# Kernel tuning notes

Measured on AMD Instinct MI355X. Metric: run time of the kernel, lower is better.

## Reference

```python
import jax, jax.numpy as jnp
import numpy as np

ALPHA = 0.2      # LeakyReLU negative slope
BN_EPS = 1e-5    # torch BatchNorm1d default eps

N_NODES = 50000
N_EDGES = 1600000
DIM_IN = 128
DIM_HID = 64
DIM_OUT = 128
NUM_HEADS = 8


def gat_layer(feat, src, dst, W, a, gamma, beta):
    """One GATLayer forward (dropout disabled, BatchNorm in training mode
    i.e. normalized with batch statistics over the node dimension)."""
    n = feat.shape[0]
    dh = W.shape[1]
    msg = feat @ W                                  # [N, dh]
    attn_src = msg @ a[:dh]                         # [N]
    attn_dst = msg @ a[dh:]                         # [N]
    scores = jax.nn.leaky_relu(attn_src[src] + attn_dst[dst], ALPHA)  # [E]
    scores = scores - scores.max()                  # global max-subtract (as in source)
    e = jnp.exp(scores)                             # [E]
    denom = jax.ops.segment_sum(e, dst, num_segments=n) + 1e-10       # [N]
    coef = e / denom[dst]                           # [E] segment-softmax
    out = jax.ops.segment_sum(msg[src] * coef[:, None], dst, num_segments=n)  # [N, dh]
    # BatchNorm1d (training-mode batch stats, biased variance)
    mean = out.mean(axis=0)
    var = out.var(axis=0)
    out = (out - mean) * jax.lax.rsqrt(var + BN_EPS) * gamma + beta
    return out


def setup_inputs() -> dict:
    key = jax.random.key(0)
    ks = jax.random.split(key, 10)
    feat = jax.random.normal(ks[0], (N_NODES, DIM_IN), dtype=jnp.float32)
    edges = jax.random.randint(ks[1], (2, N_EDGES), 0, N_NODES)

    def xavier(k, shape):
        fan_in, fan_out = shape[0], shape[-1]
        lim = np.sqrt(6.0 / (fan_in + fan_out)).astype(np.float32)
        return jax.random.uniform(k, shape, jnp.float32, -lim, lim)

    W_heads = xavier(ks[2], (NUM_HEADS, DIM_IN, DIM_HID))
    a_heads = xavier(ks[3], (NUM_HEADS, 2 * DIM_HID))
    gamma_h = jnp.ones((NUM_HEADS, DIM_HID), jnp.float32)
    beta_h = jnp.zeros((NUM_HEADS, DIM_HID), jnp.float32)
    W_out = xavier(ks[4], (NUM_HEADS * DIM_HID, DIM_OUT))
    a_out = xavier(ks[5], (2 * DIM_OUT,))
    gamma_o = jnp.ones((DIM_OUT,), jnp.float32)
    beta_o = jnp.zeros((DIM_OUT,), jnp.float32)
    W_res = xavier(ks[6], (DIM_IN, DIM_OUT))
    b_res = jnp.zeros((DIM_OUT,), jnp.float32)
    return {"feat": feat, "edges": edges, "W_heads": W_heads, "a_heads": a_heads,
            "gamma_h": gamma_h, "beta_h": beta_h, "W_out": W_out, "a_out": a_out,
            "gamma_o": gamma_o, "beta_o": beta_o, "W_res": W_res, "b_res": b_res}


def reference(feat, edges, W_heads, a_heads, gamma_h, beta_h,
              W_out, a_out, gamma_o, beta_o, W_res, b_res):
    src, dst = edges[0], edges[1]
    # python loop over a small fixed number of heads keeps peak memory low
    head_outs = [gat_layer(feat, src, dst, W_heads[h], a_heads[h], gamma_h[h], beta_h[h])
                 for h in range(NUM_HEADS)]
    x = jnp.concatenate(head_outs, axis=-1)          # [N, H*dh]
    x = gat_layer(x, src, dst, W_out, a_out, gamma_o, beta_o)  # [N, dout]
    x = x + feat @ W_res + b_res                     # residual Linear
    return x
```

## Files before the change

kernel.cpp:

```cpp
#include <hip/hip_runtime.h>
#include <math.h>

#define N_NODES 50000
#define N_EDGES 1600000
#define DIM_IN  128
#define DIM_HID 64
#define NHEADS  8
#define HDIM    (NHEADS*DIM_HID)
#define DIM_OUT 128
#define SCBLK   1024
#define HISTBLK 2048
#define NMBLK   64
#define LDK     72
#define INV_N   2e-5f
#define CSBLK   400

typedef __attribute__((ext_vector_type(2))) unsigned short us2;
typedef __attribute__((ext_vector_type(4))) unsigned short us4;
typedef __attribute__((ext_vector_type(8))) unsigned short us8;
typedef __attribute__((ext_vector_type(8))) short bf16x8;
typedef __attribute__((ext_vector_type(4))) float f32x4;

__device__ __forceinline__ float leaky(float x) { return x >= 0.f ? x : 0.2f * x; }
__device__ __forceinline__ float bf2f(unsigned short h) {
  return __uint_as_float(((unsigned)h) << 16);
}
__device__ __forceinline__ unsigned short f2bf(float f) {
  unsigned u = __float_as_uint(f);
  unsigned r = (u + 0x7fffu + ((u >> 16) & 1u)) >> 16;
  return (unsigned short)r;
}
__device__ __forceinline__ float bn_scale(float sum, float sq, float g) {
  float mean = sum * INV_N;
  float var = sq * INV_N - mean * mean;
  return g * rsqrtf(var + 1e-5f);
}

__global__ void prep_kernel(const float* __restrict__ feat, const float* __restrict__ Wh,
                            const float* __restrict__ Wres, const int* __restrict__ edst,
                            unsigned short* __restrict__ feat_bf,
                            unsigned short* __restrict__ Bt1,
                            unsigned short* __restrict__ Btr,
                            int* __restrict__ counts) {
  int b = blockIdx.x;
  if (b < 6250) {
    int i = b * 256 + threadIdx.x;
    float4 v = *reinterpret_cast<const float4*>(&feat[(size_t)i * 4]);
    us4 o;
    o[0] = f2bf(v.x); o[1] = f2bf(v.y); o[2] = f2bf(v.z); o[3] = f2bf(v.w);
    *reinterpret_cast<us4*>(&feat_bf[(size_t)i * 4]) = o;
  } else if (b < 6506) {
    int idx = (b - 6250) * 256 + threadIdx.x;
    int n = idx >> 7, k = idx & 127;
    Bt1[idx] = f2bf(Wh[(n >> 6) * (DIM_IN * DIM_HID) + k * DIM_HID + (n & 63)]);
  } else if (b < 6570) {
    int idx = (b - 6506) * 256 + threadIdx.x;
    int n = idx >> 7, k = idx & 127;
    Btr[idx] = f2bf(Wres[k * DIM_OUT + n]);
  } else {
    int bid = b - 6570;
    for (int e = bid * 256 + threadIdx.x; e < N_EDGES; e += HISTBLK * 256)
      atomicAdd(&counts[edst[e]], 1);
  }
}

__global__ __launch_bounds__(256) void foldw2_kernel(
    const float* __restrict__ W,
    const float* __restrict__ colsum, const float* __restrict__ colsq,
    const float* __restrict__ gamma, const float* __restrict__ beta,
    unsigned short* __restrict__ Bt, float* __restrict__ bias2) {
  int idx = blockIdx.x * 256 + threadIdx.x;
  int n = idx >> 9, k = idx & 511;
  float mean = colsum[k] * INV_N;
  float sc = bn_scale(colsum[k], colsq[k], gamma[k]);
  float w = W[k * DIM_OUT + n];
  Bt[idx] = f2bf(w * sc);
  float shift = beta[k] - mean * sc;
  __shared__ float red[256];
  red[threadIdx.x] = shift * w;
  __syncthreads();
#pragma unroll
  for (int off = 128; off; off >>= 1) {
    if (threadIdx.x < off) red[threadIdx.x] += red[threadIdx.x + off];
    __syncthreads();
  }
  if (threadIdx.x == 0) atomicAdd(&bias2[n], red[0]);
}

__device__ __forceinline__ void gemm_body(
    unsigned short* As, unsigned short* Bs,
    const unsigned short* __restrict__ A, const unsigned short* __restrict__ Bt,
    void* __restrict__ Cout, const float* __restrict__ bias,
    int M, int N, int K, int outbf) {
  const int tid = threadIdx.x;
  const int lane = tid & 63, wid = tid >> 6;
  const int wr = wid >> 1, wc = wid & 1;
  const int l15 = lane & 15, lhi = lane >> 4;
  const int m0 = blockIdx.y * 128, n0 = blockIdx.x * 128;
  const int srow = tid >> 3;
  const int sc8 = (tid - srow) & 7;
  f32x4 acc[4][4];
#pragma unroll
  for (int i = 0; i < 4; ++i)
#pragma unroll
    for (int j = 0; j < 4; ++j) acc[i][j] = f32x4{0.f, 0.f, 0.f, 0.f};

  for (int k0 = 0; k0 < K; k0 += 64) {
    __syncthreads();
#pragma unroll
    for (int p = 0; p < 4; ++p) {
      int row = p * 32 + srow;
      us8 va = {0, 0, 0, 0, 0, 0, 0, 0};
      int gr = m0 + row;
      if (gr < M) va = *reinterpret_cast<const us8*>(&A[(size_t)gr * K + k0 + sc8 * 8]);
      *reinterpret_cast<us8*>(&As[row * LDK + sc8 * 8]) = va;
      us8 vb = {0, 0, 0, 0, 0, 0, 0, 0};
      int gn = n0 + row;
      if (gn < N) vb = *reinterpret_cast<const us8*>(&Bt[(size_t)gn * K + k0 + sc8 * 8]);
      *reinterpret_cast<us8*>(&Bs[row * LDK + sc8 * 8]) = vb;
    }
    __syncthreads();
#pragma unroll
    for (int kk = 0; kk < 2; ++kk) {
      bf16x8 af[4], bfr[4];
#pragma unroll
      for (int i = 0; i < 4; ++i)
        af[i] = *reinterpret_cast<const bf16x8*>(&As[(wr * 64 + i * 16 + l15) * LDK + kk * 32 + lhi * 8]);
#pragma unroll
      for (int j = 0; j < 4; ++j)
        bfr[j] = *reinterpret_cast<const bf16x8*>(&Bs[(wc * 64 + j * 16 + l15) * LDK + kk * 32 + lhi * 8]);
#pragma unroll
      for (int i = 0; i < 4; ++i)
#pragma unroll
        for (int j = 0; j < 4; ++j)
          acc[i][j] = __builtin_amdgcn_mfma_f32_16x16x32_bf16(af[i], bfr[j], acc[i][j], 0, 0, 0);
    }
  }
#pragma unroll
  for (int j = 0; j < 4; ++j) {
    int col = n0 + wc * 64 + j * 16 + l15;
    float bb = bias ? bias[col] : 0.f;
#pragma unroll
    for (int i = 0; i < 4; ++i) {
      f32x4 v = acc[i][j];
#pragma unroll
      for (int t = 0; t < 4; ++t) {
        int row = m0 + wr * 64 + i * 16 + lhi * 4 + t;
        if (row < M) {
          float o = v[t] + bb;
          if (outbf) ((unsigned short*)Cout)[(size_t)row * N + col] = f2bf(o);
          else       ((float*)Cout)[(size_t)row * N + col] = o;
        }
      }
    }
  }
}

__global__ __launch_bounds__(256) void gemm1_attn_kernel(
    const unsigned short* __restrict__ A, const unsigned short* __restrict__ Bt,
    unsigned short* __restrict__ Cout, const float* __restrict__ a_heads,
    float* __restrict__ asrc, float* __restrict__ adst) {
  __shared__ unsigned short As[128 * LDK];
  __shared__ unsigned short Bs[128 * LDK];
  const int M = N_NODES, N = HDIM, K = DIM_IN;
  const int tid = threadIdx.x;
  const int lane = tid & 63, wid = tid >> 6;
  const int wr = wid >> 1, wc = wid & 1;
  const int l15 = lane & 15, lhi = lane >> 4;
  const int m0 = blockIdx.y * 128, n0 = blockIdx.x * 128;
  const int srow = tid >> 3;
  const int sc8 = (tid - srow) & 7;
  f32x4 acc[4][4];
#pragma unroll
  for (int i = 0; i < 4; ++i)
#pragma unroll
    for (int j = 0; j < 4; ++j) acc[i][j] = f32x4{0.f, 0.f, 0.f, 0.f};

  for (int k0 = 0; k0 < K; k0 += 64) {
    __syncthreads();
#pragma unroll
    for (int p = 0; p < 4; ++p) {
      int row = p * 32 + srow;
      us8 va = {0, 0, 0, 0, 0, 0, 0, 0};
      int gr = m0 + row;
      if (gr < M) va = *reinterpret_cast<const us8*>(&A[(size_t)gr * K + k0 + sc8 * 8]);
      *reinterpret_cast<us8*>(&As[row * LDK + sc8 * 8]) = va;
      us8 vb = {0, 0, 0, 0, 0, 0, 0, 0};
      int gn = n0 + row;
      if (gn < N) vb = *reinterpret_cast<const us8*>(&Bt[(size_t)gn * K + k0 + sc8 * 8]);
      *reinterpret_cast<us8*>(&Bs[row * LDK + sc8 * 8]) = vb;
    }
    __syncthreads();
#pragma unroll
    for (int kk = 0; kk < 2; ++kk) {
      bf16x8 af[4], bfr[4];
#pragma unroll
      for (int i = 0; i < 4; ++i)
        af[i] = *reinterpret_cast<const bf16x8*>(&As[(wr * 64 + i * 16 + l15) * LDK + kk * 32 + lhi * 8]);
#pragma unroll
      for (int j = 0; j < 4; ++j)
        bfr[j] = *reinterpret_cast<const bf16x8*>(&Bs[(wc * 64 + j * 16 + l15) * LDK + kk * 32 + lhi * 8]);
#pragma unroll
      for (int i = 0; i < 4; ++i)
#pragma unroll
        for (int j = 0; j < 4; ++j)
          acc[i][j] = __builtin_amdgcn_mfma_f32_16x16x32_bf16(af[i], bfr[j], acc[i][j], 0, 0, 0);
    }
  }
#pragma unroll
  for (int j = 0; j < 4; ++j) {
    int col = n0 + wc * 64 + j * 16 + l15;
#pragma unroll
    for (int i = 0; i < 4; ++i) {
      f32x4 v = acc[i][j];
#pragma unroll
      for (int t = 0; t < 4; ++t) {
        int row = m0 + wr * 64 + i * 16 + lhi * 4 + t;
        if (row < M) Cout[(size_t)row * N + col] = f2bf(v[t]);
      }
    }
  }
  const int h = blockIdx.x * 2 + wc;
  float aS[4], aD[4];
#pragma unroll
  for (int j = 0; j < 4; ++j) {
    aS[j] = a_heads[h * 128 + j * 16 + l15];
    aD[j] = a_heads[h * 128 + 64 + j * 16 + l15];
  }
#pragma unroll
  for (int i = 0; i < 4; ++i) {
#pragma unroll
    for (int t = 0; t < 4; ++t) {
      float s = 0.f, d = 0.f;
#pragma unroll
      for (int j = 0; j < 4; ++j) {
        float v = acc[i][j][t];
        s = fmaf(v, aS[j], s);
        d = fmaf(v, aD[j], d);
      }
      s += __shfl_xor(s, 1, 64); s += __shfl_xor(s, 2, 64);
      s += __shfl_xor(s, 4, 64); s += __shfl_xor(s, 8, 64);
      d += __shfl_xor(d, 1, 64); d += __shfl_xor(d, 2, 64);
      d += __shfl_xor(d, 4, 64); d += __shfl_xor(d, 8, 64);
      int row = m0 + wr * 64 + i * 16 + lhi * 4 + t;
      if (l15 == 0 && row < M) {
        asrc[(size_t)row * 8 + h] = s;
        adst[(size_t)row * 8 + h] = d;
      }
    }
  }
}

__global__ __launch_bounds__(256) void gemm_dual(
    const unsigned short* __restrict__ A0, const unsigned short* __restrict__ Bt0,
    unsigned short* __restrict__ C0, const float* __restrict__ b0,
    const float* __restrict__ a_out, float* __restrict__ asrc, float* __restrict__ adst,
    const unsigned short* __restrict__ A1, const unsigned short* __restrict__ Bt1,
    float* __restrict__ C1, const float* __restrict__ b1) {
  __shared__ unsigned short As[128 * LDK];
  __shared__ unsigned short Bs[128 * LDK];
  if (blockIdx.z == 1) {
    gemm_body(As, Bs, A1, Bt1, C1, b1, N_NODES, DIM_OUT, DIM_IN, 0);
    return;
  }
  const int M = N_NODES, N = DIM_OUT, K = HDIM;
  const int tid = threadIdx.x;
  const int lane = tid & 63, wid = tid >> 6;
  const int wr = wid >> 1, wc = wid & 1;
  const int l15 = lane & 15, lhi = lane >> 4;
  const int m0 = blockIdx.y * 128;
  const int srow = tid >> 3;
  const int sc8 = (tid - srow) & 7;
  f32x4 acc[4][4];
#pragma unroll
  for (int i = 0; i < 4; ++i)
#pragma unroll
    for (int j = 0; j < 4; ++j) acc[i][j] = f32x4{0.f, 0.f, 0.f, 0.f};

  for (int k0 = 0; k0 < K; k0 += 64) {
    __syncthreads();
#pragma unroll
    for (int p = 0; p < 4; ++p) {
      int row = p * 32 + srow;
      us8 va = {0, 0, 0, 0, 0, 0, 0, 0};
      int gr = m0 + row;
      if (gr < M) va = *reinterpret_cast<const us8*>(&A0[(size_t)gr * K + k0 + sc8 * 8]);
      *reinterpret_cast<us8*>(&As[row * LDK + sc8 * 8]) = va;
      us8 vb = {0, 0, 0, 0, 0, 0, 0, 0};
      if (row < N) vb = *reinterpret_cast<const us8*>(&Bt0[(size_t)row * K + k0 + sc8 * 8]);
      *reinterpret_cast<us8*>(&Bs[row * LDK + sc8 * 8]) = vb;
    }
    __syncthreads();
#pragma unroll
    for (int kk = 0; kk < 2; ++kk) {
      bf16x8 af[4], bfr[4];
#pragma unroll
      for (int i = 0; i < 4; ++i)
        af[i] = *reinterpret_cast<const bf16x8*>(&As[(wr * 64 + i * 16 + l15) * LDK + kk * 32 + lhi * 8]);
#pragma unroll
      for (int j = 0; j < 4; ++j)
        bfr[j] = *reinterpret_cast<const bf16x8*>(&Bs[(wc * 64 + j * 16 + l15) * LDK + kk * 32 + lhi * 8]);
#pragma unroll
      for (int i = 0; i < 4; ++i)
#pragma unroll
        for (int j = 0; j < 4; ++j)
          acc[i][j] = __builtin_amdgcn_mfma_f32_16x16x32_bf16(af[i], bfr[j], acc[i][j], 0, 0, 0);
    }
  }
#pragma unroll
  for (int j = 0; j < 4; ++j) {
    int col = wc * 64 + j * 16 + l15;
    float bb = b0[col];
#pragma unroll
    for (int i = 0; i < 4; ++i) {
      f32x4 v = acc[i][j];
#pragma unroll
      for (int t = 0; t < 4; ++t) {
        int row = m0 + wr * 64 + i * 16 + lhi * 4 + t;
        if (row < M) C0[(size_t)row * N + col] = f2bf(v[t] + bb);
      }
    }
  }
  __shared__ float att_sh[2][64][2][2];
  float aS[4], aD[4];
#pragma unroll
  for (int j = 0; j < 4; ++j) {
    int col = wc * 64 + j * 16 + l15;
    float bb = b0[col];
    aS[j] = a_out[col];
    aD[j] = a_out[128 + col];
    (void)bb;
  }
#pragma unroll
  for (int i = 0; i < 4; ++i) {
#pragma unroll
    for (int t = 0; t < 4; ++t) {
      float s = 0.f, d = 0.f;
#pragma unroll
      for (int j = 0; j < 4; ++j) {
        int col = wc * 64 + j * 16 + l15;
        float v = acc[i][j][t] + b0[col];
        s = fmaf(v, aS[j], s);
        d = fmaf(v, aD[j], d);
      }
      s += __shfl_xor(s, 1, 64); s += __shfl_xor(s, 2, 64);
      s += __shfl_xor(s, 4, 64); s += __shfl_xor(s, 8, 64);
      d += __shfl_xor(d, 1, 64); d += __shfl_xor(d, 2, 64);
      d += __shfl_xor(d, 4, 64); d += __shfl_xor(d, 8, 64);
      if (l15 == 0) {
        att_sh[wr][i * 16 + lhi * 4 + t][wc][0] = s;
        att_sh[wr][i * 16 + lhi * 4 + t][wc][1] = d;
      }
    }
  }
  __syncthreads();
  if (tid < 128) {
    int wrr = tid >> 6, r = tid & 63;
    int row = m0 + wrr * 64 + r;
    if (row < M) {
      asrc[row] = att_sh[wrr][r][0][0] + att_sh[wrr][r][1][0];
      adst[row] = att_sh[wrr][r][0][1] + att_sh[wrr][r][1][1];
    }
  }
}

__global__ __launch_bounds__(256) void nodemax_part_kernel(
    const float* __restrict__ a, const float* __restrict__ b,
    float* __restrict__ part, int total) {
  int t = threadIdx.x;
  float ms = -3.4e38f, md = -3.4e38f;
  for (int i = blockIdx.x * 256 + t; i < total; i += NMBLK * 256) {
    ms = fmaxf(ms, a[i]);
    md = fmaxf(md, b[i]);
  }
  ms = fmaxf(ms, __shfl_xor(ms, 8, 64));
  ms = fmaxf(ms, __shfl_xor(ms, 16, 64));
  ms = fmaxf(ms, __shfl_xor(ms, 32, 64));
  md = fmaxf(md, __shfl_xor(md, 8, 64));
  md = fmaxf(md, __shfl_xor(md, 16, 64));
  md = fmaxf(md, __shfl_xor(md, 32, 64));
  __shared__ float sh[4][8][2];
  int wv = t >> 6, ln = t & 63;
  if (ln < 8) { sh[wv][ln][0] = ms; sh[wv][ln][1] = md; }
  __syncthreads();
  if (t < 8) {
    float s4 = fmaxf(fmaxf(sh[0][t][0], sh[1][t][0]), fmaxf(sh[2][t][0], sh[3][t][0]));
    float d4 = fmaxf(fmaxf(sh[0][t][1], sh[1][t][1]), fmaxf(sh[2][t][1], sh[3][t][1]));
    part[blockIdx.x * 16 + t * 2] = s4;
    part[blockIdx.x * 16 + t * 2 + 1] = d4;
  }
}

__global__ void nodemax_final_kernel(const float* __restrict__ part, float* __restrict__ maxv, int H) {
  int t = threadIdx.x;
  int ch = t & 15, k = t >> 4;
  float m = -3.4e38f;
  for (int i = k; i < NMBLK; i += 4) m = fmaxf(m, part[i * 16 + ch]);
  m = fmaxf(m, __shfl_xor(m, 16, 64));
  m = fmaxf(m, __shfl_xor(m, 32, 64));
  float S = __shfl(m, (t & 7) * 2, 64);
  float D = __shfl(m, (t & 7) * 2 + 1, 64);
  if (H == 8) {
    if (t < 8) maxv[t] = S + D;
  } else {
    float Sm = S, Dm = D;
    Sm = fmaxf(Sm, __shfl_xor(Sm, 1, 64)); Sm = fmaxf(Sm, __shfl_xor(Sm, 2, 64));
    Sm = fmaxf(Sm, __shfl_xor(Sm, 4, 64));
    Dm = fmaxf(Dm, __shfl_xor(Dm, 1, 64)); Dm = fmaxf(Dm, __shfl_xor(Dm, 2, 64));
    Dm = fmaxf(Dm, __shfl_xor(Dm, 4, 64));
    if (t == 0) maxv[0] = Sm + Dm;
  }
}

__global__ __launch_bounds__(256) void scan1_kernel(
    const int* __restrict__ counts, int* __restrict__ rowptr, int* __restrict__ bsum, int n) {
  __shared__ int wsum[4];
  int b0 = blockIdx.x * 1024;
  int t = threadIdx.x;
  int lane = t & 63, w = t >> 6;
  int v[4]; int s = 0;
#pragma unroll
  for (int i = 0; i < 4; ++i) {
    int idx = b0 + t * 4 + i;
    v[i] = (idx < n) ? counts[idx] : 0;
    s += v[i];
  }
  int x = s;
#pragma unroll
  for (int off = 1; off < 64; off <<= 1) {
    int y = __shfl_up(x, off, 64);
    if (lane >= off) x += y;
  }
  if (lane == 63) wsum[w] = x;
  __syncthreads();
  int wof = 0;
  for (int i = 0; i < w; ++i) wof += wsum[i];
  int run = wof + x - s;
#pragma unroll
  for (int i = 0; i < 4; ++i) {
    int idx = b0 + t * 4 + i;
    if (idx < n) rowptr[idx] = run;
    run += v[i];
  }
  if (t == 255) bsum[blockIdx.x] = wof + x;
}

__global__ __launch_bounds__(256) void scan23_kernel(
    int* __restrict__ rowptr, const int* __restrict__ bsum, int n) {
  __shared__ int carry_sh;
  int b = blockIdx.x, t = threadIdx.x;
  if (t < 64) {
    int v = (t < b) ? bsum[t] : 0;
#pragma unroll
    for (int off = 32; off; off >>= 1) v += __shfl_xor(v, off, 64);
    if (t == 0) carry_sh = v;
  }
  __syncthreads();
  int carry = carry_sh;
  int i0 = b * 1024;
#pragma unroll
  for (int q = 0; q < 4; ++q) {
    int i = i0 + q * 256 + t;
    if (i < n) rowptr[i] += carry;
  }
  if (b == gridDim.x - 1 && t == 0) rowptr[n] = N_EDGES;
}

__global__ __launch_bounds__(256) void scatter_kernel(
    const int* __restrict__ esrc, const int* __restrict__ edst,
    const int* __restrict__ rowptr, int* __restrict__ cursor,
    int* __restrict__ colsrc, int E) {
  for (int e = blockIdx.x * blockDim.x + threadIdx.x; e < E; e += gridDim.x * blockDim.x) {
    int d = edst[e];
    int pos = rowptr[d] + atomicAdd(&cursor[d], 1);
    colsrc[pos] = esrc[e];
  }
}

__global__ __launch_bounds__(256) void agg1_kernel(
    const unsigned short* __restrict__ msg, const float* __restrict__ asrc,
    const float* __restrict__ adst, const float* __restrict__ maxv,
    const int* __restrict__ rowptr, const int* __restrict__ colsrc,
    unsigned short* __restrict__ out) {
  int wv = threadIdx.x >> 6, l = threadIdx.x & 63;
  int n = blockIdx.x * 4 + wv;
  const int h = l >> 3;
  const int eloc = l & 7;
  const int hbase = l & 56;
  float M = maxv[h];
  float ad = adst[(size_t)n * 8 + h];
  int e0 = rowptr[n], e1 = rowptr[n + 1];
  float acc[8];
#pragma unroll
  for (int j = 0; j < 8; ++j) acc[j] = 0.f;
  float ds = 0.f;
  int base = e0;
  for (; base + 8 <= e1; base += 8) {
    int sreg = colsrc[base + eloc];
    float x = asrc[(size_t)sreg * 8 + h] + ad;
    x = x >= 0.f ? x : 0.2f * x;
    float creg = __expf(x - M);
#pragma unroll
    for (int e = 0; e < 8; ++e) {
      float c = __shfl(creg, hbase | e, 64);
      int s = __shfl(sreg, e, 64);
      ds += c;
      us8 m = *reinterpret_cast<const us8*>(&msg[(size_t)s * HDIM + l * 8]);
#pragma unroll
      for (int j = 0; j < 8; ++j) acc[j] = fmaf(bf2f(m[j]), c, acc[j]);
    }
  }
  if (base < e1) {
    int cnt = e1 - base;
    int sreg = 0; float creg = 0.f;
    if (eloc < cnt) {
      sreg = colsrc[base + eloc];
      float x = asrc[(size_t)sreg * 8 + h] + ad;
      x = x >= 0.f ? x : 0.2f * x;
      creg = __expf(x - M);
    }
    for (int e = 0; e < cnt; ++e) {
      float c = __shfl(creg, hbase | e, 64);
      int s = __shfl(sreg, e, 64);
      ds += c;
      us8 m = *reinterpret_cast<const us8*>(&msg[(size_t)s * HDIM + l * 8]);
#pragma unroll
      for (int j = 0; j < 8; ++j) acc[j] = fmaf(bf2f(m[j]), c, acc[j]);
    }
  }
  float inv = 1.0f / (ds + 1e-10f);
  us8 o;
#pragma unroll
  for (int j = 0; j < 8; ++j) o[j] = f2bf(acc[j] * inv);
  *reinterpret_cast<us8*>(&out[(size_t)n * HDIM + l * 8]) = o;
}

__global__ __launch_bounds__(256) void agg2_kernel(
    const unsigned short* __restrict__ msg, const float* __restrict__ asrc,
    const float* __restrict__ adst, const float* __restrict__ maxv,
    const int* __restrict__ rowptr, const int* __restrict__ colsrc,
    float* __restrict__ out) {
  int wv = threadIdx.x >> 6, ln = threadIdx.x & 63;
  int n = blockIdx.x * 4 + wv;
  float M = maxv[0];
  float ad = adst[n];
  int e0 = rowptr[n], e1 = rowptr[n + 1];
  float a0 = 0.f, a1 = 0.f, ds = 0.f;
  for (int base = e0; base < e1; base += 64) {
    int cnt = min(64, e1 - base);
    int s_reg = 0; float c_reg = 0.f;
    if (ln < cnt) {
      s_reg = colsrc[base + ln];
      float x = asrc[s_reg] + ad;
      x = x >= 0.f ? x : 0.2f * x;
      c_reg = __expf(x - M);
    }
    int e = 0;
    for (; e + 4 <= cnt; e += 4) {
      int s0 = __shfl(s_reg, e, 64),     s1 = __shfl(s_reg, e + 1, 64);
      int s2 = __shfl(s_reg, e + 2, 64), s3 = __shfl(s_reg, e + 3, 64);
      float c0 = __shfl(c_reg, e, 64),     c1 = __shfl(c_reg, e + 1, 64);
      float c2 = __shfl(c_reg, e + 2, 64), c3 = __shfl(c_reg, e + 3, 64);
      us2 m0 = *reinterpret_cast<const us2*>(&msg[(size_t)s0 * 128 + 2 * ln]);
      us2 m1 = *reinterpret_cast<const us2*>(&msg[(size_t)s1 * 128 + 2 * ln]);
      us2 m2 = *reinterpret_cast<const us2*>(&msg[(size_t)s2 * 128 + 2 * ln]);
      us2 m3 = *reinterpret_cast<const us2*>(&msg[(size_t)s3 * 128 + 2 * ln]);
      ds += (c0 + c1) + (c2 + c3);
      a0 = fmaf(bf2f(m0[0]), c0, a0); a1 = fmaf(bf2f(m0[1]), c0, a1);
      a0 = fmaf(bf2f(m1[0]), c1, a0); a1 = fmaf(bf2f(m1[1]), c1, a1);
      a0 = fmaf(bf2f(m2[0]), c2, a0); a1 = fmaf(bf2f(m2[1]), c2, a1);
      a0 = fmaf(bf2f(m3[0]), c3, a0); a1 = fmaf(bf2f(m3[1]), c3, a1);
    }
    for (; e < cnt; ++e) {
      int s = __shfl(s_reg, e, 64);
      float c = __shfl(c_reg, e, 64);
      us2 m = *reinterpret_cast<const us2*>(&msg[(size_t)s * 128 + 2 * ln]);
      ds += c;
      a0 = fmaf(bf2f(m[0]), c, a0);
      a1 = fmaf(bf2f(m[1]), c, a1);
    }
  }
  float inv = 1.0f / (ds + 1e-10f);
  float2 r; r.x = a0 * inv; r.y = a1 * inv;
  *reinterpret_cast<float2*>(&out[(size_t)n * 128 + 2 * ln]) = r;
}

__global__ __launch_bounds__(256) void colstats_bf512_kernel(
    const unsigned short* __restrict__ X, float* __restrict__ sums,
    float* __restrict__ sqs, int M) {
  int tid = threadIdx.x;
  int cg = tid & 63;
  int wv = tid >> 6;
  int rows = (M + gridDim.x - 1) / gridDim.x;
  int r0 = blockIdx.x * rows;
  int r1 = min(M, r0 + rows);
  float s[8], q[8];
#pragma unroll
  for (int j = 0; j < 8; ++j) { s[j] = 0.f; q[j] = 0.f; }
  for (int r = r0 + wv; r < r1; r += 4) {
    us8 v = *reinterpret_cast<const us8*>(&X[(size_t)r * 512 + cg * 8]);
#pragma unroll
    for (int j = 0; j < 8; ++j) {
      float f = bf2f(v[j]);
      s[j] += f; q[j] = fmaf(f, f, q[j]);
    }
  }
  __shared__ float shs[3][512];
  __shared__ float shq[3][512];
  if (wv > 0) {
#pragma unroll
    for (int j = 0; j < 8; ++j) {
      shs[wv - 1][cg * 8 + j] = s[j];
      shq[wv - 1][cg * 8 + j] = q[j];
    }
  }
  __syncthreads();
  if (wv == 0) {
#pragma unroll
    for (int j = 0; j < 8; ++j) {
      int c = cg * 8 + j;
      atomicAdd(&sums[c], s[j] + shs[0][c] + shs[1][c] + shs[2][c]);
      atomicAdd(&sqs[c],  q[j] + shq[0][c] + shq[1][c] + shq[2][c]);
    }
  }
}

__global__ __launch_bounds__(256) void colstats_f128_kernel(
    const float* __restrict__ X, float* __restrict__ sums,
    float* __restrict__ sqs, int M) {
  int tid = threadIdx.x;
  int g = tid & 31;
  int slot = tid >> 5;
  int rows = (M + gridDim.x - 1) / gridDim.x;
  int r0 = blockIdx.x * rows;
  int r1 = min(M, r0 + rows);
  float s[4] = {0.f, 0.f, 0.f, 0.f}, q[4] = {0.f, 0.f, 0.f, 0.f};
  for (int r = r0 + slot; r < r1; r += 8) {
    float4 v = *reinterpret_cast<const float4*>(&X[(size_t)r * 128 + g * 4]);
    s[0] += v.x; q[0] = fmaf(v.x, v.x, q[0]);
    s[1] += v.y; q[1] = fmaf(v.y, v.y, q[1]);
    s[2] += v.z; q[2] = fmaf(v.z, v.z, q[2]);
    s[3] += v.w; q[3] = fmaf(v.w, v.w, q[3]);
  }
#pragma unroll
  for (int j = 0; j < 4; ++j) {
    s[j] += __shfl_xor(s[j], 32, 64);
    q[j] += __shfl_xor(q[j], 32, 64);
  }
  __shared__ float shs[3][128];
  __shared__ float shq[3][128];
  int wv = tid >> 6, ln = tid & 63;
  if (wv > 0 && ln < 32) {
#pragma unroll
    for (int j = 0; j < 4; ++j) {
      shs[wv - 1][g * 4 + j] = s[j];
      shq[wv - 1][g * 4 + j] = q[j];
    }
  }
  __syncthreads();
  if (wv == 0 && ln < 32) {
#pragma unroll
    for (int j = 0; j < 4; ++j) {
      int c = g * 4 + j;
      atomicAdd(&sums[c], s[j] + shs[0][c] + shs[1][c] + shs[2][c]);
      atomicAdd(&sqs[c],  q[j] + shq[0][c] + shq[1][c] + shq[2][c]);
    }
  }
}

__global__ void final_kernel(float* __restrict__ out, const float* __restrict__ resid,
                             const float* __restrict__ colsum, const float* __restrict__ colsq,
                             const float* __restrict__ gamma, const float* __restrict__ beta,
                             int total) {
  for (int i = blockIdx.x * blockDim.x + threadIdx.x; i < total; i += gridDim.x * blockDim.x) {
    int c = i & 127;
    float mean = colsum[c] * INV_N;
    float sc = bn_scale(colsum[c], colsq[c], gamma[c]);
    float sh = beta[c] - mean * sc;
    out[i] = fmaf(out[i], sc, sh) + resid[i];
  }
}

extern "C" void kernel_launch(void* const* d_in, const int* in_sizes, int n_in,
                              void* d_out, int out_size, void* d_ws, size_t ws_size,
                              hipStream_t stream) {
  const float* feat    = (const float*)d_in[0];
  const int*   edges   = (const int*)d_in[1];
  const int*   esrc    = edges;
  const int*   edst    = edges + N_EDGES;
  const float* W_heads = (const float*)d_in[2];
  const float* a_heads = (const float*)d_in[3];
  const float* gamma_h = (const float*)d_in[4];
  const float* beta_h  = (const float*)d_in[5];
  const float* W_out   = (const float*)d_in[6];
  const float* a_out   = (const float*)d_in[7];
  const float* gamma_o = (const float*)d_in[8];
  const float* beta_o  = (const float*)d_in[9];
  const float* W_res   = (const float*)d_in[10];
  const float* b_res   = (const float*)d_in[11];
  float* out = (float*)d_out;

  char* ws = (char*)d_ws;
  size_t off = 0;
  auto alloc = [&](size_t bytes) {
    void* p = ws + off;
    off = (off + bytes + 255) & ~(size_t)255;
    return p;
  };
  unsigned short* msg1    = (unsigned short*)alloc((size_t)N_NODES * HDIM * 2);
  unsigned short* out1_bf = (unsigned short*)alloc((size_t)N_NODES * HDIM * 2);
  unsigned short* feat_bf = (unsigned short*)alloc((size_t)N_NODES * DIM_IN * 2);
  float*    resid  = (float*)alloc((size_t)N_NODES * DIM_OUT * 4);
  float*    asrc1  = (float*)alloc((size_t)N_NODES * NHEADS * 4);
  float*    adst1  = (float*)alloc((size_t)N_NODES * NHEADS * 4);
  int*      counts = (int*)alloc((size_t)N_NODES * 4);
  int*      cursor = (int*)alloc((size_t)N_NODES * 4);
  float*    bias2  = (float*)alloc(DIM_OUT * 4);
  int*      rowptr = (int*)alloc((size_t)(N_NODES + 1) * 4);
  int*      colsrc = (int*)alloc((size_t)N_EDGES * 4);
  int*      bsum   = (int*)alloc(64 * 4);
  float*    partmx = (float*)alloc((size_t)NMBLK * 16 * 4);
  float*    maxv1  = (float*)alloc(8 * 4);
  float*    maxv2  = (float*)alloc(4);
  float*    colsum = (float*)alloc(HDIM * 4);
  float*    colsq  = (float*)alloc(HDIM * 4);
  unsigned short* Bt1 = (unsigned short*)alloc((size_t)HDIM * DIM_IN * 2);
  unsigned short* Bt2 = (unsigned short*)alloc((size_t)DIM_OUT * HDIM * 2);
  unsigned short* Btr = (unsigned short*)alloc((size_t)DIM_OUT * DIM_IN * 2);
  unsigned short* msg2 = msg1;
  float* asrc2 = asrc1; float* adst2 = adst1;
  (void)n_in; (void)in_sizes; (void)out_size; (void)ws_size;

  hipMemsetAsync(counts, 0, (char*)rowptr - (char*)counts, stream);
  hipMemsetAsync(colsum, 0, 4096, stream);

  prep_kernel<<<6570 + HISTBLK, 256, 0, stream>>>(feat, W_heads, W_res, edst,
                                                  feat_bf, Bt1, Btr, counts);

  dim3 g1(HDIM / 128, (N_NODES + 127) / 128);
  gemm1_attn_kernel<<<g1, 256, 0, stream>>>(feat_bf, Bt1, msg1, a_heads, asrc1, adst1);
  nodemax_part_kernel<<<NMBLK, 256, 0, stream>>>(asrc1, adst1, partmx, N_NODES * 8);
  nodemax_final_kernel<<<1, 64, 0, stream>>>(partmx, maxv1, 8);

  int nsb = (N_NODES + 1023) / 1024;
  scan1_kernel<<<nsb, 256, 0, stream>>>(counts, rowptr, bsum, N_NODES);
  scan23_kernel<<<nsb, 256, 0, stream>>>(rowptr, bsum, N_NODES);

  scatter_kernel<<<SCBLK, 256, 0, stream>>>(esrc, edst, rowptr, cursor, colsrc, N_EDGES);
  agg1_kernel<<<N_NODES / 4, 256, 0, stream>>>(msg1, asrc1, adst1, maxv1, rowptr, colsrc, out1_bf);

  colstats_bf512_kernel<<<CSBLK, 256, 0, stream>>>(out1_bf, colsum, colsq, N_NODES);
  foldw2_kernel<<<DIM_OUT * HDIM / 256, 256, 0, stream>>>(W_out, colsum, colsq,
                                                          gamma_h, beta_h, Bt2, bias2);

  dim3 g2d(1, (N_NODES + 127) / 128, 2);
  gemm_dual<<<g2d, 256, 0, stream>>>(out1_bf, Bt2, msg2, bias2, a_out, asrc2, adst2,
                                     feat_bf, Btr, resid, b_res);
  nodemax_part_kernel<<<NMBLK, 256, 0, stream>>>(asrc2, adst2, partmx, N_NODES);
  nodemax_final_kernel<<<1, 64, 0, stream>>>(partmx, maxv2, 1);

  agg2_kernel<<<N_NODES / 4, 256, 0, stream>>>(msg2, asrc2, adst2, maxv2, rowptr, colsrc, out);

  hipMemsetAsync(colsum, 0, 4096, stream);
  colstats_f128_kernel<<<CSBLK, 256, 0, stream>>>(out, colsum, colsq, N_NODES);
  final_kernel<<<2048, 256, 0, stream>>>(out, resid, colsum, colsq, gamma_o, beta_o,
                                         N_NODES * DIM_OUT);
}
```

Measured before the change: 716.8 us.

## Fuse attention max reduction into GEMM epilogues and widen agg2 loads

```diff
diff --git a/kernel.cpp b/kernel.cpp
--- a/kernel.cpp
+++ b/kernel.cpp
@@ -10,7 +10,7 @@
 #define DIM_OUT 128
 #define SCBLK   1024
 #define HISTBLK 2048
-#define NMBLK   64
+#define NBY     391
 #define LDK     72
 #define INV_N   2e-5f
 #define CSBLK   400
@@ -159,7 +159,7 @@
 __global__ __launch_bounds__(256) void gemm1_attn_kernel(
     const unsigned short* __restrict__ A, const unsigned short* __restrict__ Bt,
     unsigned short* __restrict__ Cout, const float* __restrict__ a_heads,
-    float* __restrict__ asrc, float* __restrict__ adst) {
+    float* __restrict__ asrc, float* __restrict__ adst, float* __restrict__ partmx) {
   __shared__ unsigned short As[128 * LDK];
   __shared__ unsigned short Bs[128 * LDK];
   const int M = N_NODES, N = HDIM, K = DIM_IN;
@@ -227,6 +227,7 @@
     aS[j] = a_heads[h * 128 + j * 16 + l15];
     aD[j] = a_heads[h * 128 + 64 + j * 16 + l15];
   }
+  float ms = -3.4e38f, md = -3.4e38f;
 #pragma unroll
   for (int i = 0; i < 4; ++i) {
 #pragma unroll
@@ -246,8 +247,19 @@
       if (l15 == 0 && row < M) {
         asrc[(size_t)row * 8 + h] = s;
         adst[(size_t)row * 8 + h] = d;
+        ms = fmaxf(ms, s); md = fmaxf(md, d);
       }
     }
+  }
+  ms = fmaxf(ms, __shfl_xor(ms, 16, 64)); ms = fmaxf(ms, __shfl_xor(ms, 32, 64));
+  md = fmaxf(md, __shfl_xor(md, 16, 64)); md = fmaxf(md, __shfl_xor(md, 32, 64));
+  __shared__ float shmx[2][2][2];
+  if (lane == 0) { shmx[wr][wc][0] = ms; shmx[wr][wc][1] = md; }
+  __syncthreads();
+  if (tid < 2) {
+    size_t base = ((size_t)blockIdx.y * 4 + blockIdx.x) * 4 + tid * 2;
+    partmx[base]     = fmaxf(shmx[0][tid][0], shmx[1][tid][0]);
+    partmx[base + 1] = fmaxf(shmx[0][tid][1], shmx[1][tid][1]);
   }
 }
 
@@ -255,6 +267,7 @@
     const unsigned short* __restrict__ A0, const unsigned short* __restrict__ Bt0,
     unsigned short* __restrict__ C0, const float* __restrict__ b0,
     const float* __restrict__ a_out, float* __restrict__ asrc, float* __restrict__ adst,
+    float* __restrict__ part2,
     const unsigned short* __restrict__ A1, const unsigned short* __restrict__ Bt1,
     float* __restrict__ C1, const float* __restrict__ b1) {
   __shared__ unsigned short As[128 * LDK];
@@ -326,10 +339,8 @@
 #pragma unroll
   for (int j = 0; j < 4; ++j) {
     int col = wc * 64 + j * 16 + l15;
-    float bb = b0[col];
     aS[j] = a_out[col];
     aD[j] = a_out[128 + col];
-    (void)bb;
   }
 #pragma unroll
   for (int i = 0; i < 4; ++i) {
@@ -354,61 +365,60 @@
     }
   }
   __syncthreads();
+  float s2 = -3.4e38f, d2 = -3.4e38f;
   if (tid < 128) {
     int wrr = tid >> 6, r = tid & 63;
     int row = m0 + wrr * 64 + r;
     if (row < M) {
-      asrc[row] = att_sh[wrr][r][0][0] + att_sh[wrr][r][1][0];
-      adst[row] = att_sh[wrr][r][0][1] + att_sh[wrr][r][1][1];
-    }
-  }
-}
-
-__global__ __launch_bounds__(256) void nodemax_part_kernel(
-    const float* __restrict__ a, const float* __restrict__ b,
-    float* __restrict__ part, int total) {
+      float sv = att_sh[wrr][r][0][0] + att_sh[wrr][r][1][0];
+      float dv = att_sh[wrr][r][0][1] + att_sh[wrr][r][1][1];
+      asrc[row] = sv; adst[row] = dv;
+      s2 = sv; d2 = dv;
+    }
+  }
+#pragma unroll
+  for (int off = 32; off; off >>= 1) {
+    s2 = fmaxf(s2, __shfl_xor(s2, off, 64));
+    d2 = fmaxf(d2, __shfl_xor(d2, off, 64));
+  }
+  __shared__ float shm2[2][2];
+  int wvid = tid >> 6, lnn = tid & 63;
+  if (wvid < 2 && lnn == 0) { shm2[wvid][0] = s2; shm2[wvid][1] = d2; }
+  __syncthreads();
+  if (tid == 0) {
+    part2[blockIdx.y * 2]     = fmaxf(shm2[0][0], shm2[1][0]);
+    part2[blockIdx.y * 2 + 1] = fmaxf(shm2[0][1], shm2[1][1]);
+  }
+}
+
+__global__ void nodemax_final_kernel(const float* __restrict__ part, float* __restrict__ maxv,
+                                     int H, int nby) {
   int t = threadIdx.x;
-  float ms = -3.4e38f, md = -3.4e38f;
-  for (int i = blockIdx.x * 256 + t; i < total; i += NMBLK * 256) {
-    ms = fmaxf(ms, a[i]);
-    md = fmaxf(md, b[i]);
-  }
-  ms = fmaxf(ms, __shfl_xor(ms, 8, 64));
-  ms = fmaxf(ms, __shfl_xor(ms, 16, 64));
-  ms = fmaxf(ms, __shfl_xor(ms, 32, 64));
-  md = fmaxf(md, __shfl_xor(md, 8, 64));
-  md = fmaxf(md, __shfl_xor(md, 16, 64));
-  md = fmaxf(md, __shfl_xor(md, 32, 64));
-  __shared__ float sh[4][8][2];
-  int wv = t >> 6, ln = t & 63;
-  if (ln < 8) { sh[wv][ln][0] = ms; sh[wv][ln][1] = md; }
-  __syncthreads();
-  if (t < 8) {
-    float s4 = fmaxf(fmaxf(sh[0][t][0], sh[1][t][0]), fmaxf(sh[2][t][0], sh[3][t][0]));
-    float d4 = fmaxf(fmaxf(sh[0][t][1], sh[1][t][1]), fmaxf(sh[2][t][1], sh[3][t][1]));
-    part[blockIdx.x * 16 + t * 2] = s4;
-    part[blockIdx.x * 16 + t * 2 + 1] = d4;
-  }
-}
-
-__global__ void nodemax_final_kernel(const float* __restrict__ part, float* __restrict__ maxv, int H) {
-  int t = threadIdx.x;
-  int ch = t & 15, k = t >> 4;
-  float m = -3.4e38f;
-  for (int i = k; i < NMBLK; i += 4) m = fmaxf(m, part[i * 16 + ch]);
-  m = fmaxf(m, __shfl_xor(m, 16, 64));
-  m = fmaxf(m, __shfl_xor(m, 32, 64));
-  float S = __shfl(m, (t & 7) * 2, 64);
-  float D = __shfl(m, (t & 7) * 2 + 1, 64);
   if (H == 8) {
-    if (t < 8) maxv[t] = S + D;
+    int h = t >> 3, j = t & 7;
+    float S = -3.4e38f, D = -3.4e38f;
+    for (int by = j; by < nby; by += 8) {
+      int base = (by * 4 + (h >> 1)) * 4 + (h & 1) * 2;
+      S = fmaxf(S, part[base]);
+      D = fmaxf(D, part[base + 1]);
+    }
+    S = fmaxf(S, __shfl_xor(S, 1, 64)); S = fmaxf(S, __shfl_xor(S, 2, 64));
+    S = fmaxf(S, __shfl_xor(S, 4, 64));
+    D = fmaxf(D, __shfl_xor(D, 1, 64)); D = fmaxf(D, __shfl_xor(D, 2, 64));
+    D = fmaxf(D, __shfl_xor(D, 4, 64));
+    if (j == 0) maxv[h] = S + D;
   } else {
-    float Sm = S, Dm = D;
-    Sm = fmaxf(Sm, __shfl_xor(Sm, 1, 64)); Sm = fmaxf(Sm, __shfl_xor(Sm, 2, 64));
-    Sm = fmaxf(Sm, __shfl_xor(Sm, 4, 64));
-    Dm = fmaxf(Dm, __shfl_xor(Dm, 1, 64)); Dm = fmaxf(Dm, __shfl_xor(Dm, 2, 64));
-    Dm = fmaxf(Dm, __shfl_xor(Dm, 4, 64));
-    if (t == 0) maxv[0] = Sm + Dm;
+    float S = -3.4e38f, D = -3.4e38f;
+    for (int by = t; by < nby; by += 64) {
+      S = fmaxf(S, part[by * 2]);
+      D = fmaxf(D, part[by * 2 + 1]);
+    }
+#pragma unroll
+    for (int off = 32; off; off >>= 1) {
+      S = fmaxf(S, __shfl_xor(S, off, 64));
+      D = fmaxf(D, __shfl_xor(D, off, 64));
+    }
+    if (t == 0) maxv[0] = S + D;
   }
 }
 
@@ -542,10 +552,12 @@
     float* __restrict__ out) {
   int wv = threadIdx.x >> 6, ln = threadIdx.x & 63;
   int n = blockIdx.x * 4 + wv;
+  int half = ln >> 5, q = ln & 31;
   float M = maxv[0];
   float ad = adst[n];
   int e0 = rowptr[n], e1 = rowptr[n + 1];
-  float a0 = 0.f, a1 = 0.f, ds = 0.f;
+  float acc[4] = {0.f, 0.f, 0.f, 0.f};
+  float ds = 0.f;
   for (int base = e0; base < e1; base += 64) {
     int cnt = min(64, e1 - base);
     int s_reg = 0; float c_reg = 0.f;
@@ -555,34 +567,44 @@
       x = x >= 0.f ? x : 0.2f * x;
       c_reg = __expf(x - M);
     }
+    int cnt4 = cnt & ~3;
     int e = 0;
-    for (; e + 4 <= cnt; e += 4) {
-      int s0 = __shfl(s_reg, e, 64),     s1 = __shfl(s_reg, e + 1, 64);
-      int s2 = __shfl(s_reg, e + 2, 64), s3 = __shfl(s_reg, e + 3, 64);
-      float c0 = __shfl(c_reg, e, 64),     c1 = __shfl(c_reg, e + 1, 64);
-      float c2 = __shfl(c_reg, e + 2, 64), c3 = __shfl(c_reg, e + 3, 64);
-      us2 m0 = *reinterpret_cast<const us2*>(&msg[(size_t)s0 * 128 + 2 * ln]);
-      us2 m1 = *reinterpret_cast<const us2*>(&msg[(size_t)s1 * 128 + 2 * ln]);
-      us2 m2 = *reinterpret_cast<const us2*>(&msg[(size_t)s2 * 128 + 2 * ln]);
-      us2 m3 = *reinterpret_cast<const us2*>(&msg[(size_t)s3 * 128 + 2 * ln]);
-      ds += (c0 + c1) + (c2 + c3);
-      a0 = fmaf(bf2f(m0[0]), c0, a0); a1 = fmaf(bf2f(m0[1]), c0, a1);
-      a0 = fmaf(bf2f(m1[0]), c1, a0); a1 = fmaf(bf2f(m1[1]), c1, a1);
-      a0 = fmaf(bf2f(m2[0]), c2, a0); a1 = fmaf(bf2f(m2[1]), c2, a1);
-      a0 = fmaf(bf2f(m3[0]), c3, a0); a1 = fmaf(bf2f(m3[1]), c3, a1);
-    }
-    for (; e < cnt; ++e) {
-      int s = __shfl(s_reg, e, 64);
-      float c = __shfl(c_reg, e, 64);
-      us2 m = *reinterpret_cast<const us2*>(&msg[(size_t)s * 128 + 2 * ln]);
+    for (; e < cnt4; e += 4) {
+      int sA = __shfl(s_reg, e + half, 64);
+      int sB = __shfl(s_reg, e + 2 + half, 64);
+      float cA = __shfl(c_reg, e + half, 64);
+      float cB = __shfl(c_reg, e + 2 + half, 64);
+      us4 mA = *reinterpret_cast<const us4*>(&msg[(size_t)sA * 128 + q * 4]);
+      us4 mB = *reinterpret_cast<const us4*>(&msg[(size_t)sB * 128 + q * 4]);
+      ds += cA + cB;
+#pragma unroll
+      for (int j = 0; j < 4; ++j) {
+        acc[j] = fmaf(bf2f(mA[j]), cA, acc[j]);
+        acc[j] = fmaf(bf2f(mB[j]), cB, acc[j]);
+      }
+    }
+    for (; e < cnt; e += 2) {
+      int idx = e + half;
+      int idc = idx < cnt ? idx : 0;
+      int s = __shfl(s_reg, idc, 64);
+      float c = __shfl(c_reg, idc, 64);
+      if (idx >= cnt) c = 0.f;
+      us4 m = *reinterpret_cast<const us4*>(&msg[(size_t)s * 128 + q * 4]);
       ds += c;
-      a0 = fmaf(bf2f(m[0]), c, a0);
-      a1 = fmaf(bf2f(m[1]), c, a1);
-    }
-  }
-  float inv = 1.0f / (ds + 1e-10f);
-  float2 r; r.x = a0 * inv; r.y = a1 * inv;
-  *reinterpret_cast<float2*>(&out[(size_t)n * 128 + 2 * ln]) = r;
+#pragma unroll
+      for (int j = 0; j < 4; ++j) acc[j] = fmaf(bf2f(m[j]), c, acc[j]);
+    }
+  }
+  ds += __shfl_xor(ds, 32, 64);
+#pragma unroll
+  for (int j = 0; j < 4; ++j) acc[j] += __shfl_xor(acc[j], 32, 64);
+  if (half == 0) {
+    float inv = 1.0f / (ds + 1e-10f);
+    float4 r;
+    r.x = acc[0] * inv; r.y = acc[1] * inv;
+    r.z = acc[2] * inv; r.w = acc[3] * inv;
+    *reinterpret_cast<float4*>(&out[(size_t)n * 128 + q * 4]) = r;
+  }
 }
 
 __global__ __launch_bounds__(256) void colstats_bf512_kernel(
@@ -713,17 +735,20 @@
   float*    resid  = (float*)alloc((size_t)N_NODES * DIM_OUT * 4);
   float*    asrc1  = (float*)alloc((size_t)N_NODES * NHEADS * 4);
   float*    adst1  = (float*)alloc((size_t)N_NODES * NHEADS * 4);
-  int*      counts = (int*)alloc((size_t)N_NODES * 4);
-  int*      cursor = (int*)alloc((size_t)N_NODES * 4);
-  float*    bias2  = (float*)alloc(DIM_OUT * 4);
-  int*      rowptr = (int*)alloc((size_t)(N_NODES + 1) * 4);
-  int*      colsrc = (int*)alloc((size_t)N_EDGES * 4);
-  int*      bsum   = (int*)alloc(64 * 4);
-  float*    partmx = (float*)alloc((size_t)NMBLK * 16 * 4);
-  float*    maxv1  = (float*)alloc(8 * 4);
-  float*    maxv2  = (float*)alloc(4);
-  float*    colsum = (float*)alloc(HDIM * 4);
-  float*    colsq  = (float*)alloc(HDIM * 4);
+  int*      counts  = (int*)alloc((size_t)N_NODES * 4);
+  int*      cursor  = (int*)alloc((size_t)N_NODES * 4);
+  float*    bias2   = (float*)alloc(DIM_OUT * 4);
+  float*    colsum1 = (float*)alloc(HDIM * 4);
+  float*    colsq1  = (float*)alloc(HDIM * 4);
+  float*    colsum2 = (float*)alloc(DIM_OUT * 4);
+  float*    colsq2  = (float*)alloc(DIM_OUT * 4);
+  int*      rowptr  = (int*)alloc((size_t)(N_NODES + 1) * 4);
+  int*      colsrc  = (int*)alloc((size_t)N_EDGES * 4);
+  int*      bsum    = (int*)alloc(64 * 4);
+  float*    partmx1 = (float*)alloc((size_t)NBY * 4 * 4 * 4);
+  float*    partmx2 = (float*)alloc((size_t)NBY * 2 * 4);
+  float*    maxv1   = (float*)alloc(8 * 4);
+  float*    maxv2   = (float*)alloc(4);
   unsigned short* Bt1 = (unsigned short*)alloc((size_t)HDIM * DIM_IN * 2);
   unsigned short* Bt2 = (unsigned short*)alloc((size_t)DIM_OUT * HDIM * 2);
   unsigned short* Btr = (unsigned short*)alloc((size_t)DIM_OUT * DIM_IN * 2);
@@ -732,15 +757,13 @@
   (void)n_in; (void)in_sizes; (void)out_size; (void)ws_size;
 
   hipMemsetAsync(counts, 0, (char*)rowptr - (char*)counts, stream);
-  hipMemsetAsync(colsum, 0, 4096, stream);
 
   prep_kernel<<<6570 + HISTBLK, 256, 0, stream>>>(feat, W_heads, W_res, edst,
                                                   feat_bf, Bt1, Btr, counts);
 
-  dim3 g1(HDIM / 128, (N_NODES + 127) / 128);
-  gemm1_attn_kernel<<<g1, 256, 0, stream>>>(feat_bf, Bt1, msg1, a_heads, asrc1, adst1);
-  nodemax_part_kernel<<<NMBLK, 256, 0, stream>>>(asrc1, adst1, partmx, N_NODES * 8);
-  nodemax_final_kernel<<<1, 64, 0, stream>>>(partmx, maxv1, 8);
+  dim3 g1(HDIM / 128, NBY);
+  gemm1_attn_kernel<<<g1, 256, 0, stream>>>(feat_bf, Bt1, msg1, a_heads, asrc1, adst1, partmx1);
+  nodemax_final_kernel<<<1, 64, 0, stream>>>(partmx1, maxv1, 8, NBY);
 
   int nsb = (N_NODES + 1023) / 1024;
   scan1_kernel<<<nsb, 256, 0, stream>>>(counts, rowptr, bsum, N_NODES);
@@ -749,20 +772,18 @@
   scatter_kernel<<<SCBLK, 256, 0, stream>>>(esrc, edst, rowptr, cursor, colsrc, N_EDGES);
   agg1_kernel<<<N_NODES / 4, 256, 0, stream>>>(msg1, asrc1, adst1, maxv1, rowptr, colsrc, out1_bf);
 
-  colstats_bf512_kernel<<<CSBLK, 256, 0, stream>>>(out1_bf, colsum, colsq, N_NODES);
-  foldw2_kernel<<<DIM_OUT * HDIM / 256, 256, 0, stream>>>(W_out, colsum, colsq,
+  colstats_bf512_kernel<<<CSBLK, 256, 0, stream>>>(out1_bf, colsum1, colsq1, N_NODES);
+  foldw2_kernel<<<DIM_OUT * HDIM / 256, 256, 0, stream>>>(W_out, colsum1, colsq1,
                                                           gamma_h, beta_h, Bt2, bias2);
 
-  dim3 g2d(1, (N_NODES + 127) / 128, 2);
-  gemm_dual<<<g2d, 256, 0, stream>>>(out1_bf, Bt2, msg2, bias2, a_out, asrc2, adst2,
+  dim3 g2d(1, NBY, 2);
+  gemm_dual<<<g2d, 256, 0, stream>>>(out1_bf, Bt2, msg2, bias2, a_out, asrc2, adst2, partmx2,
                                      feat_bf, Btr, resid, b_res);
-  nodemax_part_kernel<<<NMBLK, 256, 0, stream>>>(asrc2, adst2, partmx, N_NODES);
-  nodemax_final_kernel<<<1, 64, 0, stream>>>(partmx, maxv2, 1);
+  nodemax_final_kernel<<<1, 64, 0, stream>>>(partmx2, maxv2, 1, NBY);
 
   agg2_kernel<<<N_NODES / 4, 256, 0, stream>>>(msg2, asrc2, adst2, maxv2, rowptr, colsrc, out);
 
-  hipMemsetAsync(colsum, 0, 4096, stream);
-  colstats_f128_kernel<<<CSBLK, 256, 0, stream>>>(out, colsum, colsq, N_NODES);
-  final_kernel<<<2048, 256, 0, stream>>>(out, resid, colsum, colsq, gamma_o, beta_o,
+  colstats_f128_kernel<<<CSBLK, 256, 0, stream>>>(out, colsum2, colsq2, N_NODES);
+  final_kernel<<<2048, 256, 0, stream>>>(out, resid, colsum2, colsq2, gamma_o, beta_o,
                                          N_NODES * DIM_OUT);
 }
```

Result: no change. 714.3 us (-0.4%).
